# Performance work log

Measured on AMD Instinct MI355X. Metric: run time of the kernel, lower is better.

## Reference

```python
import jax, jax.numpy as jnp
import numpy as np

D_MODEL = 1024
D_STATE = 16
D_CONV = 4
EXPAND = 2
D_INNER = EXPAND * D_MODEL
BATCH = 4
SEQLEN = 2048
LN_EPS = 1e-5


def setup_inputs() -> dict:
    key = jax.random.key(0)
    ks = jax.random.split(key, 10)
    x = jax.random.normal(ks[0], (BATCH, SEQLEN, D_MODEL), dtype=jnp.float32)
    # parameters (torch Linear weights stored transposed here: [in, out])
    in_proj_w = jax.random.normal(ks[1], (D_MODEL, 2 * D_INNER), jnp.float32) * (1.0 / np.sqrt(D_MODEL))
    conv_w = jax.random.normal(ks[2], (D_INNER, 1, D_CONV), jnp.float32) * (1.0 / np.sqrt(D_CONV))  # OIH, depthwise
    conv_b = jax.random.normal(ks[3], (D_INNER,), jnp.float32) * 0.02
    x_proj_w = jax.random.normal(ks[4], (D_INNER, 2 * D_STATE), jnp.float32) * (1.0 / np.sqrt(D_INNER))
    dt_proj_w = jax.random.normal(ks[5], (D_INNER, D_INNER), jnp.float32) * (1.0 / np.sqrt(D_INNER))
    dt_proj_b = jax.random.normal(ks[6], (D_INNER,), jnp.float32) * 0.02
    # A = arange(1..d_state) repeated over d_inner; store log
    A_log = jnp.log(jnp.tile(jnp.arange(1, D_STATE + 1, dtype=jnp.float32)[None, :], (D_INNER, 1)))
    D_param = jnp.ones((D_INNER,), jnp.float32)
    out_proj_w = jax.random.normal(ks[7], (D_INNER, D_MODEL), jnp.float32) * (1.0 / np.sqrt(D_INNER))
    ln_gamma = jnp.ones((D_MODEL,), jnp.float32)
    ln_beta = jnp.zeros((D_MODEL,), jnp.float32)
    return {
        'x': x, 'ln_gamma': ln_gamma, 'ln_beta': ln_beta,
        'in_proj_w': in_proj_w, 'conv_w': conv_w, 'conv_b': conv_b,
        'x_proj_w': x_proj_w, 'dt_proj_w': dt_proj_w, 'dt_proj_b': dt_proj_b,
        'A_log': A_log, 'D_param': D_param, 'out_proj_w': out_proj_w,
    }


def _selective_scan(u, delta, A, Bm):
    # u, delta: [B, L, d_inner]; Bm: [B, L, d_state]; A: [d_inner, d_state]
    batch, _, d_inner = u.shape
    d_state = A.shape[1]

    def step(h, inp):
        u_t, d_t, b_t = inp  # [B,di], [B,di], [B,ds]
        dA = jnp.exp(d_t[..., None] * A)                      # [B,di,ds]
        h = h * dA + (u_t * d_t)[..., None] * b_t[:, None, :]  # [B,di,ds]
        return h, h.sum(-1)                                    # y_t: [B,di]

    h0 = jnp.zeros((batch, d_inner, d_state), u.dtype)
    xs = (jnp.swapaxes(u, 0, 1), jnp.swapaxes(delta, 0, 1), jnp.swapaxes(Bm, 0, 1))
    _, ys = jax.lax.scan(step, h0, xs)  # ys: [L,B,di]
    return jnp.swapaxes(ys, 0, 1)


def reference(x, ln_gamma, ln_beta, in_proj_w, conv_w, conv_b, x_proj_w,
              dt_proj_w, dt_proj_b, A_log, D_param, out_proj_w):
    residual = x
    # LayerNorm
    mu = x.mean(-1, keepdims=True)
    var = jnp.mean(jnp.square(x - mu), axis=-1, keepdims=True)
    xn = (x - mu) * jax.lax.rsqrt(var + LN_EPS) * ln_gamma + ln_beta
    # in_proj, split into u (ssm path) and z (gate)
    xz = xn @ in_proj_w                      # [B,L,2*di]
    u, z = jnp.split(xz, 2, axis=-1)
    # causal depthwise conv1d (torch pads d_conv-1 both sides then slices -> left-pad only)
    uc = jnp.swapaxes(u, 1, 2)               # [B,di,L]
    uc = jax.lax.conv_general_dilated(
        uc, conv_w, window_strides=(1,), padding=[(D_CONV - 1, 0)],
        dimension_numbers=('NCH', 'OIH', 'NCH'), feature_group_count=D_INNER,
    ) + conv_b[None, :, None]
    u = jax.nn.silu(jnp.swapaxes(uc, 1, 2))  # [B,L,di]
    # projections; note: first d_state chunk of x_dbl is discarded (overwritten by dt_proj)
    x_dbl = u @ x_proj_w                     # [B,L,2*ds]
    Bm = x_dbl[..., D_STATE:]
    delta = jax.nn.softplus(u @ dt_proj_w + dt_proj_b)
    A = -jnp.exp(A_log)
    y = _selective_scan(u, delta, A, Bm)
    y = y + u * D_param
    y = y * jax.nn.silu(z)
    return y @ out_proj_w + residual
```

## Files before the change

### kernel.cpp

```cpp
#include <hip/hip_runtime.h>

typedef unsigned short u16;
typedef unsigned int   u32;

#define D_MODEL 1024
#define D_INNER 2048
#define D_STATE 16
#define SEQLEN  2048
#define BATCH   4
#define NROWS   (BATCH*SEQLEN)
#define CHUNK   128
#define NCHUNK  (SEQLEN/CHUNK)

__device__ __forceinline__ float b2f(u16 v){
  union { u32 i; float f; } u; u.i = ((u32)v) << 16; return u.f;
}
__device__ __forceinline__ u16 f2b(float f){
  union { float f; u32 i; } u; u.f = f;
  u32 x = u.i;
  return (u16)((x + 0x7fffu + ((x >> 16) & 1u)) >> 16);
}
__device__ __forceinline__ float h2f(u16 v){
  _Float16 h; __builtin_memcpy(&h, &v, 2); return (float)h;
}
__device__ __forceinline__ u16 f2h(float f){
  _Float16 h = (_Float16)f; u16 v; __builtin_memcpy(&v, &h, 2); return v;
}

typedef __bf16 bf16x8 __attribute__((ext_vector_type(8)));
typedef float  f32x4  __attribute__((ext_vector_type(4)));

__device__ __forceinline__ void async16(u16* lds, const u16* g){
  __builtin_amdgcn_global_load_lds(
      (const __attribute__((address_space(1))) void*)g,
      (__attribute__((address_space(3))) void*)lds,
      16, 0, 0);
}

__global__ __launch_bounds__(256) void wcvt_t_kernel(
    const float* __restrict__ W, u16* __restrict__ Bt, int Kd, int Nd)
{
  __shared__ u16 tile[32][33];
  const int n0 = blockIdx.x*32, k0 = blockIdx.y*32;
  const int tx = threadIdx.x & 31, ty = threadIdx.x >> 5;
  #pragma unroll
  for (int i=0;i<32;i+=8)
    tile[ty+i][tx] = f2b(W[(size_t)(k0+ty+i)*Nd + n0+tx]);
  __syncthreads();
  #pragma unroll
  for (int i=0;i<32;i+=8)
    Bt[(size_t)(n0+ty+i)*Kd + k0+tx] = tile[tx][ty+i];
}

__global__ __launch_bounds__(256) void wxcvt_kernel(
    const float* __restrict__ Wx, u16* __restrict__ Wxt)
{
  const int k = blockIdx.x*256 + threadIdx.x;
  #pragma unroll
  for (int n=0;n<16;n++)
    Wxt[n*D_INNER + k] = f2b(Wx[(size_t)k*32 + 16 + n]);
}

__global__ __launch_bounds__(256) void ln_kernel(
    const float* __restrict__ x, const float* __restrict__ g,
    const float* __restrict__ be, u16* __restrict__ xn)
{
  const int row = blockIdx.x;
  const float* xr = x + (size_t)row * D_MODEL;
  const int tid = threadIdx.x;
  float v[4]; float s = 0.f, s2 = 0.f;
  #pragma unroll
  for (int j=0;j<4;j++){
    float f = xr[tid + 256*j];
    v[j] = f; s += f; s2 += f*f;
  }
  #pragma unroll
  for (int o=32;o>0;o>>=1){ s += __shfl_down(s,o); s2 += __shfl_down(s2,o); }
  __shared__ float sh[8];
  const int wave = tid>>6, lane = tid&63;
  if (lane==0){ sh[wave]=s; sh[4+wave]=s2; }
  __syncthreads();
  const float ts  = sh[0]+sh[1]+sh[2]+sh[3];
  const float ts2 = sh[4]+sh[5]+sh[6]+sh[7];
  const float mu  = ts * (1.f/D_MODEL);
  const float var = ts2 * (1.f/D_MODEL) - mu*mu;
  const float rstd = rsqrtf(var + 1e-5f);
  u16* xo = xn + (size_t)row * D_MODEL;
  #pragma unroll
  for (int j=0;j<4;j++){
    int i = tid + 256*j;
    xo[i] = f2b((v[j]-mu)*rstd * g[i] + be[i]);
  }
}

template<int EPI>
__global__ __launch_bounds__(256) void gemm_bk64(
    const u16* __restrict__ A, const u16* __restrict__ Bt,
    const float* __restrict__ bias, const float* __restrict__ resid,
    void* __restrict__ outv, int M, int N, int K, int gx, int gy)
{
  __shared__ __align__(16) u16 As[2*128*32];
  __shared__ __align__(16) u16 Bs[2*128*32];
  const int tid  = threadIdx.x;
  const int wave = tid >> 6, lane = tid & 63;
  const int quad = lane >> 4, l16 = lane & 15;

  const int lid = blockIdx.x;
  const int xcd = lid & 7, q = lid >> 3;
  const int cpx = gx >> 3;
  const int qd  = q / gy;
  const int bx  = xcd*cpx + qd;
  const int by  = q - qd*gy;
  const int m0 = by*128, n0 = bx*128;
  const int wm = (wave & 1)*64, wn = (wave >> 1)*64;

  const int srow = wave*32 + (lane >> 2);
  const int gcol = ((lane & 3) ^ ((lane >> 3) & 3)) * 8;
  const u16* pA = A  + (size_t)(m0 + srow)*K + gcol;
  const u16* pB = Bt + (size_t)(n0 + srow)*K + gcol;
  u16* lA = &As[(wave*32)*32];
  u16* lB = &Bs[(wave*32)*32];

  const int sw   = quad ^ ((l16 >> 1) & 3);
  const int aoff = (wm + l16)*64 + sw*16;
  const int boff = (wn + l16)*64 + sw*16;

  f32x4 acc[4][4];
  #pragma unroll
  for (int i=0;i<4;i++)
    #pragma unroll
    for (int j=0;j<4;j++) acc[i][j] = (f32x4){0.f,0.f,0.f,0.f};

  for (int k0 = 0; k0 < K; k0 += 64) {
    __syncthreads();
    async16(lA,               pA + k0);
    async16(lA + 16*32,       pA + (size_t)16*K + k0);
    async16(lA + 4096,        pA + k0 + 32);
    async16(lA + 4096+16*32,  pA + (size_t)16*K + k0 + 32);
    async16(lB,               pB + k0);
    async16(lB + 16*32,       pB + (size_t)16*K + k0);
    async16(lB + 4096,        pB + k0 + 32);
    async16(lB + 4096+16*32,  pB + (size_t)16*K + k0 + 32);
    __syncthreads();

    #pragma unroll
    for (int ks=0; ks<2; ks++){
      bf16x8 afr[4], bfr[4];
      #pragma unroll
      for (int mf=0; mf<4; mf++)
        afr[mf] = *reinterpret_cast<const bf16x8*>((const char*)As + ks*8192 + aoff + mf*1024);
      #pragma unroll
      for (int nf=0; nf<4; nf++)
        bfr[nf] = *reinterpret_cast<const bf16x8*>((const char*)Bs + ks*8192 + boff + nf*1024);
      #pragma unroll
      for (int mf=0; mf<4; mf++)
        #pragma unroll
        for (int nf=0; nf<4; nf++)
          acc[mf][nf] = __builtin_amdgcn_mfma_f32_16x16x32_bf16(afr[mf], bfr[nf], acc[mf][nf], 0, 0, 0);
    }
  }

  #pragma unroll
  for (int mf=0; mf<4; mf++){
    #pragma unroll
    for (int nf=0; nf<4; nf++){
      const int col = n0 + wn + nf*16 + l16;
      #pragma unroll
      for (int j=0;j<4;j++){
        const int row = m0 + wm + mf*16 + quad*4 + j;
        float v = acc[mf][nf][j];
        if (EPI == 1) {
          v += bias[col];
          v = (v > 20.f) ? v : log1pf(__expf(v));
          ((u16*)outv)[(size_t)row*N + col] = f2h(v);
        } else if (EPI == 2) {
          v += resid[(size_t)row*N + col];
          ((float*)outv)[(size_t)row*N + col] = v;
        } else {
          ((u16*)outv)[(size_t)row*N + col] = f2b(v);
        }
      }
    }
  }
}

__global__ __launch_bounds__(256) void conv_silu_kernel(
    const u16* __restrict__ xz, const float* __restrict__ cw,
    const float* __restrict__ cb, u16* __restrict__ u)
{
  const int idx = blockIdx.x*256 + threadIdx.x;
  const int c0 = (idx & 255) * 8;
  const int bt = idx >> 8;
  const int t  = bt & (SEQLEN-1);
  float acc[8];
  #pragma unroll
  for (int j=0;j<8;j++) acc[j] = cb[c0+j];
  #pragma unroll
  for (int k=0;k<4;k++){
    if (t - 3 + k >= 0){
      bf16x8 xv = *reinterpret_cast<const bf16x8*>(xz + (size_t)(bt-3+k)*4096 + c0);
      #pragma unroll
      for (int j=0;j<8;j++)
        acc[j] = fmaf(cw[(c0+j)*4 + k], (float)xv[j], acc[j]);
    }
  }
  u16 o[8];
  #pragma unroll
  for (int j=0;j<8;j++){
    float sv = acc[j] / (1.f + __expf(-acc[j]));
    o[j] = f2b(sv);
  }
  __builtin_memcpy(u + (size_t)bt*D_INNER + c0, o, 16);
}

__global__ __launch_bounds__(256) void xproj_kernel(
    const u16* __restrict__ u, const u16* __restrict__ Wxt, float* __restrict__ Bm)
{
  const int wave = threadIdx.x >> 6, lane = threadIdx.x & 63;
  const int m = blockIdx.x*4 + wave;
  const int n = lane & 15, kq = lane >> 4;
  const u16* ur = u   + (size_t)m*D_INNER + kq*512;
  const u16* wr = Wxt + (size_t)n*D_INNER + kq*512;
  float acc = 0.f;
  #pragma unroll 4
  for (int i=0;i<512;i+=8){
    bf16x8 uv = *reinterpret_cast<const bf16x8*>(ur + i);
    bf16x8 wv = *reinterpret_cast<const bf16x8*>(wr + i);
    #pragma unroll
    for (int j=0;j<8;j++) acc = fmaf((float)uv[j], (float)wv[j], acc);
  }
  acc += __shfl_xor(acc, 16);
  acc += __shfl_xor(acc, 32);
  if (lane < 16) Bm[(size_t)m*16 + n] = acc;
}

__global__ __launch_bounds__(256) void scan_partial(
    const u16* __restrict__ uu, const u16* __restrict__ delta16,
    const float* __restrict__ Bm, const float* __restrict__ Alog,
    float* __restrict__ hend, float* __restrict__ sumdt)
{
  const int b = blockIdx.y, ch = blockIdx.z;
  const int c = blockIdx.x*256 + threadIdx.x;
  const int row0 = b*SEQLEN + ch*CHUNK;
  float A[16], h[16];
  #pragma unroll
  for (int s=0;s<16;s++){ A[s] = -__expf(Alog[c*16+s]); h[s]=0.f; }
  __shared__ float Bsh[CHUNK*16];
  const float* src = Bm + (size_t)row0*16;
  #pragma unroll
  for (int j=0;j<8;j++) Bsh[threadIdx.x + 256*j] = src[threadIdx.x + 256*j];
  __syncthreads();

  float S = 0.f;
  float dta[8], uva[8], dtb[8], uvb[8];
  #pragma unroll
  for (int j=0;j<8;j++){
    size_t r = (size_t)(row0+j);
    dta[j] = h2f(delta16[r*D_INNER+c]);
    uva[j] = b2f(uu[r*D_INNER+c]);
  }
  #pragma unroll 1
  for (int g=0; g<CHUNK; g+=16){
    #pragma unroll
    for (int j=0;j<8;j++){
      int tl = g+8+j; tl = tl < CHUNK ? tl : CHUNK-1;
      size_t r = (size_t)(row0+tl);
      dtb[j] = h2f(delta16[r*D_INNER+c]);
      uvb[j] = b2f(uu[r*D_INNER+c]);
    }
    #pragma unroll
    for (int j=0;j<8;j++){
      float dt=dta[j], uv=uva[j]; S += dt; float xv=dt*uv;
      const float* Bt = &Bsh[(g+j)*16];
      #pragma unroll
      for (int s=0;s<16;s++) h[s] = fmaf(h[s], __expf(dt*A[s]), xv*Bt[s]);
    }
    #pragma unroll
    for (int j=0;j<8;j++){
      int tl = g+16+j; tl = tl < CHUNK ? tl : CHUNK-1;
      size_t r = (size_t)(row0+tl);
      dta[j] = h2f(delta16[r*D_INNER+c]);
      uva[j] = b2f(uu[r*D_INNER+c]);
    }
    #pragma unroll
    for (int j=0;j<8;j++){
      float dt=dtb[j], uv=uvb[j]; S += dt; float xv=dt*uv;
      const float* Bt = &Bsh[(g+8+j)*16];
      #pragma unroll
      for (int s=0;s<16;s++) h[s] = fmaf(h[s], __expf(dt*A[s]), xv*Bt[s]);
    }
  }
  const size_t base = ((size_t)(b*NCHUNK+ch)*16)*D_INNER + c;
  #pragma unroll
  for (int s=0;s<16;s++) hend[base + (size_t)s*D_INNER] = h[s];
  sumdt[(size_t)(b*NCHUNK+ch)*D_INNER + c] = S;
}

__global__ __launch_bounds__(256) void scan_combine(
    const float* __restrict__ hend, const float* __restrict__ sumdt,
    const float* __restrict__ Alog, float* __restrict__ hin)
{
  const int b = blockIdx.y;
  const int c = blockIdx.x*256 + threadIdx.x;
  float A[16], h[16];
  #pragma unroll
  for (int s=0;s<16;s++){ A[s] = -__expf(Alog[c*16+s]); h[s]=0.f; }
  #pragma unroll 1
  for (int k=0;k<NCHUNK;k++){
    const size_t base = ((size_t)(b*NCHUNK+k)*16)*D_INNER + c;
    #pragma unroll
    for (int s=0;s<16;s++) hin[base + (size_t)s*D_INNER] = h[s];
    const float S = sumdt[(size_t)(b*NCHUNK+k)*D_INNER + c];
    #pragma unroll
    for (int s=0;s<16;s++)
      h[s] = fmaf(h[s], __expf(S*A[s]), hend[base + (size_t)s*D_INNER]);
  }
}

__global__ __launch_bounds__(256) void scan_final(
    const u16* __restrict__ uu, const u16* __restrict__ delta16,
    const float* __restrict__ Bm, const u16* __restrict__ xz,
    const float* __restrict__ Alog, const float* __restrict__ Dpar,
    const float* __restrict__ hin, u16* __restrict__ yg)
{
  const int b = blockIdx.y, ch = blockIdx.z;
  const int c = blockIdx.x*256 + threadIdx.x;
  const int row0 = b*SEQLEN + ch*CHUNK;
  float A[16], h[16];
  const size_t base = ((size_t)(b*NCHUNK+ch)*16)*D_INNER + c;
  #pragma unroll
  for (int s=0;s<16;s++){
    A[s] = -__expf(Alog[c*16+s]);
    h[s] = hin[base + (size_t)s*D_INNER];
  }
  const float Dc = Dpar[c];
  __shared__ float Bsh[CHUNK*16];
  const float* src = Bm + (size_t)row0*16;
  #pragma unroll
  for (int j=0;j<8;j++) Bsh[threadIdx.x + 256*j] = src[threadIdx.x + 256*j];
  __syncthreads();

  float dta[8], uva[8], zva[8], dtb[8], uvb[8], zvb[8];
  #pragma unroll
  for (int j=0;j<8;j++){
    size_t r = (size_t)(row0+j);
    dta[j] = h2f(delta16[r*D_INNER+c]);
    uva[j] = b2f(uu[r*D_INNER+c]);
    zva[j] = b2f(xz[r*4096 + D_INNER + c]);
  }
  #pragma unroll 1
  for (int g=0; g<CHUNK; g+=16){
    #pragma unroll
    for (int j=0;j<8;j++){
      int tl = g+8+j; tl = tl < CHUNK ? tl : CHUNK-1;
      size_t r = (size_t)(row0+tl);
      dtb[j] = h2f(delta16[r*D_INNER+c]);
      uvb[j] = b2f(uu[r*D_INNER+c]);
      zvb[j] = b2f(xz[r*4096 + D_INNER + c]);
    }
    #pragma unroll
    for (int j=0;j<8;j++){
      float dt=dta[j], uv=uva[j], zv=zva[j];
      float xv=dt*uv, y=0.f;
      const float* Bt = &Bsh[(g+j)*16];
      #pragma unroll
      for (int s=0;s<16;s++){
        h[s] = fmaf(h[s], __expf(dt*A[s]), xv*Bt[s]);
        y += h[s];
      }
      y = fmaf(uv, Dc, y);
      float gz = zv/(1.f+__expf(-zv));
      yg[(size_t)(row0+g+j)*D_INNER + c] = f2b(y*gz);
    }
    #pragma unroll
    for (int j=0;j<8;j++){
      int tl = g+16+j; tl = tl < CHUNK ? tl : CHUNK-1;
      size_t r = (size_t)(row0+tl);
      dta[j] = h2f(delta16[r*D_INNER+c]);
      uva[j] = b2f(uu[r*D_INNER+c]);
      zva[j] = b2f(xz[r*4096 + D_INNER + c]);
    }
    #pragma unroll
    for (int j=0;j<8;j++){
      float dt=dtb[j], uv=uvb[j], zv=zvb[j];
      float xv=dt*uv, y=0.f;
      const float* Bt = &Bsh[(g+8+j)*16];
      #pragma unroll
      for (int s=0;s<16;s++){
        h[s] = fmaf(h[s], __expf(dt*A[s]), xv*Bt[s]);
        y += h[s];
      }
      y = fmaf(uv, Dc, y);
      float gz = zv/(1.f+__expf(-zv));
      yg[(size_t)(row0+g+8+j)*D_INNER + c] = f2b(y*gz);
    }
  }
}

extern "C" void kernel_launch(void* const* d_in, const int* in_sizes, int n_in,
                              void* d_out, int out_size, void* d_ws, size_t ws_size,
                              hipStream_t stream)
{
  const float* x    = (const float*)d_in[0];
  const float* lng  = (const float*)d_in[1];
  const float* lnb  = (const float*)d_in[2];
  const float* W1   = (const float*)d_in[3];
  const float* cw   = (const float*)d_in[4];
  const float* cb   = (const float*)d_in[5];
  const float* Wx   = (const float*)d_in[6];
  const float* Wdt  = (const float*)d_in[7];
  const float* dtb  = (const float*)d_in[8];
  const float* Alog = (const float*)d_in[9];
  const float* Dpar = (const float*)d_in[10];
  const float* Wout = (const float*)d_in[11];

  char* ws = (char*)d_ws;
  u16*   dlt   = (u16*)(ws);
  u16*   xn    = (u16*)(ws);
  u16*   xz    = (u16*)(ws + (32llu<<20));
  u16*   uu    = (u16*)(ws + (96llu<<20));
  float* Bm    = (float*)(ws + (128llu<<20));
  u16*   W1t   = (u16*)(ws + (129llu<<20));
  u16*   Wdtt  = (u16*)(ws + (137llu<<20));
  u16*   Woutt = (u16*)(ws + (145llu<<20));
  u16*   yg    = (u16*)(ws + (149llu<<20));
  float* hend  = (float*)(ws + (181llu<<20));
  float* sumdt = (float*)(ws + (189llu<<20));
  float* hin   = (float*)(ws + (190llu<<20));
  u16*   Wxt   = (u16*)(ws + (198llu<<20));

  wcvt_t_kernel<<<dim3(2*D_INNER/32, D_MODEL/32), 256, 0, stream>>>(W1,  W1t,  D_MODEL, 2*D_INNER);
  wcvt_t_kernel<<<dim3(D_INNER/32,  D_INNER/32), 256, 0, stream>>>(Wdt, Wdtt, D_INNER, D_INNER);
  wcvt_t_kernel<<<dim3(D_MODEL/32,  D_INNER/32), 256, 0, stream>>>(Wout,Woutt,D_INNER, D_MODEL);
  wxcvt_kernel<<<D_INNER/256, 256, 0, stream>>>(Wx, Wxt);

  ln_kernel<<<NROWS, 256, 0, stream>>>(x, lng, lnb, xn);

  {
    const int gx = 2*D_INNER/128, gy = NROWS/128;
    gemm_bk64<0><<<gx*gy, 256, 0, stream>>>(
        xn, W1t, nullptr, nullptr, (void*)xz, NROWS, 2*D_INNER, D_MODEL, gx, gy);
  }

  conv_silu_kernel<<<(NROWS*D_INNER/8)/256, 256, 0, stream>>>(xz, cw, cb, uu);

  xproj_kernel<<<NROWS/4, 256, 0, stream>>>(uu, Wxt, Bm);

  {
    const int gx = D_INNER/128, gy = NROWS/128;
    gemm_bk64<1><<<gx*gy, 256, 0, stream>>>(
        uu, Wdtt, dtb, nullptr, (void*)dlt, NROWS, D_INNER, D_INNER, gx, gy);
  }

  scan_partial<<<dim3(D_INNER/256, BATCH, NCHUNK), 256, 0, stream>>>(
      uu, dlt, Bm, Alog, hend, sumdt);
  scan_combine<<<dim3(D_INNER/256, BATCH), 256, 0, stream>>>(
      hend, sumdt, Alog, hin);
  scan_final<<<dim3(D_INNER/256, BATCH, NCHUNK), 256, 0, stream>>>(
      uu, dlt, Bm, xz, Alog, Dpar, hin, yg);

  {
    const int gx = D_MODEL/128, gy = NROWS/128;
    gemm_bk64<2><<<gx*gy, 256, 0, stream>>>(
        yg, Woutt, nullptr, x, d_out, NROWS, D_MODEL, D_INNER, gx, gy);
  }

  (void)in_sizes; (void)n_in; (void)out_size; (void)ws_size;
}
```

Baseline: 783.3 us.

## Replace 128x128 GEMM with 256x256 tile, 4-stage async pipelined kernel

Replaces the double-sync 128x128 bf16 MFMA GEMM with a 256x256 tile, 512-thread kernel. It uses a 4-deep ring of LDS buffers filled by async global-to-LDS loads issued three k-steps ahead, with s_setprio around MFMA bursts and split A-fragment loads to interleave LDS reads with compute. The goal is to raise data reuse per tile and hide global memory latency behind MFMA work. The cost is larger LDS use (128KB), lower occupancy, and fewer blocks for the smaller GEMMs (128 blocks for out_proj), which may underfill the GPU.

```diff
diff --git a/kernel.cpp b/kernel.cpp
--- a/kernel.cpp
+++ b/kernel.cpp
@@ -94,80 +94,124 @@
 }
 
 template<int EPI>
-__global__ __launch_bounds__(256) void gemm_bk64(
+__global__ __launch_bounds__(512) void gemm256(
     const u16* __restrict__ A, const u16* __restrict__ Bt,
     const float* __restrict__ bias, const float* __restrict__ resid,
     void* __restrict__ outv, int M, int N, int K, int gx, int gy)
 {
-  __shared__ __align__(16) u16 As[2*128*32];
-  __shared__ __align__(16) u16 Bs[2*128*32];
+  __shared__ __align__(16) u16 As[4*8192];
+  __shared__ __align__(16) u16 Bs[4*8192];
   const int tid  = threadIdx.x;
   const int wave = tid >> 6, lane = tid & 63;
   const int quad = lane >> 4, l16 = lane & 15;
+  const int wm = wave >> 2, wn = wave & 3;
 
   const int lid = blockIdx.x;
-  const int xcd = lid & 7, q = lid >> 3;
-  const int cpx = gx >> 3;
-  const int qd  = q / gy;
-  const int bx  = xcd*cpx + qd;
-  const int by  = q - qd*gy;
-  const int m0 = by*128, n0 = bx*128;
-  const int wm = (wave & 1)*64, wn = (wave >> 1)*64;
-
-  const int srow = wave*32 + (lane >> 2);
-  const int gcol = ((lane & 3) ^ ((lane >> 3) & 3)) * 8;
-  const u16* pA = A  + (size_t)(m0 + srow)*K + gcol;
-  const u16* pB = Bt + (size_t)(n0 + srow)*K + gcol;
-  u16* lA = &As[(wave*32)*32];
-  u16* lB = &Bs[(wave*32)*32];
-
-  const int sw   = quad ^ ((l16 >> 1) & 3);
-  const int aoff = (wm + l16)*64 + sw*16;
-  const int boff = (wn + l16)*64 + sw*16;
-
-  f32x4 acc[4][4];
-  #pragma unroll
-  for (int i=0;i<4;i++)
+  int bx, by;
+  if ((gx & 7) == 0) {
+    const int xcd = lid & 7, q = lid >> 3;
+    const int cpx = gx >> 3;
+    const int qd  = q / gy;
+    bx = xcd*cpx + qd;
+    by = q - qd*gy;
+  } else {
+    bx = lid / gy;
+    by = lid - bx*gy;
+  }
+  const int m0 = by*256, n0 = bx*256;
+
+  const int gl   = (tid & 3) ^ ((tid >> 3) & 3);
+  const int srow = tid >> 2;
+  const u16* sA0 = A  + (size_t)(m0 + srow)*K       + gl*8;
+  const u16* sA1 = A  + (size_t)(m0 + 128 + srow)*K + gl*8;
+  const u16* sB0 = Bt + (size_t)(n0 + srow)*K       + gl*8;
+  const u16* sB1 = Bt + (size_t)(n0 + 128 + srow)*K + gl*8;
+  u16* dA = As + wave*512;
+  u16* dB = Bs + wave*512;
+
+  const int swz = quad ^ ((l16 >> 1) & 3);
+  const char* aBase = (const char*)As + (wm*128 + l16)*64 + swz*16;
+  const char* bBase = (const char*)Bs + (wn*64  + l16)*64 + swz*16;
+
+  f32x4 acc[8][4];
+  #pragma unroll
+  for (int i=0;i<8;i++)
     #pragma unroll
     for (int j=0;j<4;j++) acc[i][j] = (f32x4){0.f,0.f,0.f,0.f};
 
-  for (int k0 = 0; k0 < K; k0 += 64) {
-    __syncthreads();
-    async16(lA,               pA + k0);
-    async16(lA + 16*32,       pA + (size_t)16*K + k0);
-    async16(lA + 4096,        pA + k0 + 32);
-    async16(lA + 4096+16*32,  pA + (size_t)16*K + k0 + 32);
-    async16(lB,               pB + k0);
-    async16(lB + 16*32,       pB + (size_t)16*K + k0);
-    async16(lB + 4096,        pB + k0 + 32);
-    async16(lB + 4096+16*32,  pB + (size_t)16*K + k0 + 32);
-    __syncthreads();
-
-    #pragma unroll
-    for (int ks=0; ks<2; ks++){
-      bf16x8 afr[4], bfr[4];
-      #pragma unroll
-      for (int mf=0; mf<4; mf++)
-        afr[mf] = *reinterpret_cast<const bf16x8*>((const char*)As + ks*8192 + aoff + mf*1024);
-      #pragma unroll
-      for (int nf=0; nf<4; nf++)
-        bfr[nf] = *reinterpret_cast<const bf16x8*>((const char*)Bs + ks*8192 + boff + nf*1024);
-      #pragma unroll
-      for (int mf=0; mf<4; mf++)
-        #pragma unroll
-        for (int nf=0; nf<4; nf++)
-          acc[mf][nf] = __builtin_amdgcn_mfma_f32_16x16x32_bf16(afr[mf], bfr[nf], acc[mf][nf], 0, 0, 0);
-    }
-  }
-
-  #pragma unroll
-  for (int mf=0; mf<4; mf++){
+  const int KT = K >> 5;
+
+  #pragma unroll
+  for (int p=0;p<3;p++){
+    const int ko = p*32;
+    u16* da = dA + p*8192; u16* db = dB + p*8192;
+    async16(da,        sA0 + ko);
+    async16(da + 4096, sA1 + ko);
+    async16(db,        sB0 + ko);
+    async16(db + 4096, sB1 + ko);
+  }
+  asm volatile("s_waitcnt vmcnt(8)" ::: "memory");
+  __builtin_amdgcn_s_barrier();
+  __builtin_amdgcn_sched_barrier(0);
+
+  for (int kt = 0; kt < KT; ++kt){
+    const int c = kt & 3;
+    const char* aT = aBase + c*16384;
+    const char* bT = bBase + c*16384;
+
+    bf16x8 af[4], bfr[4];
+    #pragma unroll
+    for (int mf=0;mf<4;mf++) af[mf]  = *(const bf16x8*)(aT + mf*1024);
+    #pragma unroll
+    for (int nf=0;nf<4;nf++) bfr[nf] = *(const bf16x8*)(bT + nf*1024);
+    {
+      int k3 = kt + 3; k3 = (k3 < KT) ? k3 : (KT-1);
+      const int b3 = (kt + 3) & 3;
+      const int ko = k3*32;
+      u16* da = dA + b3*8192; u16* db = dB + b3*8192;
+      async16(da,        sA0 + ko);
+      async16(da + 4096, sA1 + ko);
+      async16(db,        sB0 + ko);
+      async16(db + 4096, sB1 + ko);
+    }
+    __builtin_amdgcn_s_barrier();
+    asm volatile("s_waitcnt lgkmcnt(0)" ::: "memory");
+    __builtin_amdgcn_sched_barrier(0);
+    __builtin_amdgcn_s_setprio(1);
+    #pragma unroll
+    for (int mf=0;mf<4;mf++)
+      #pragma unroll
+      for (int nf=0;nf<4;nf++)
+        acc[mf][nf] = __builtin_amdgcn_mfma_f32_16x16x32_bf16(af[mf], bfr[nf], acc[mf][nf], 0, 0, 0);
+    __builtin_amdgcn_s_setprio(0);
+    __builtin_amdgcn_s_barrier();
+
+    bf16x8 ag[4];
+    #pragma unroll
+    for (int mf=0;mf<4;mf++) ag[mf] = *(const bf16x8*)(aT + (4+mf)*1024);
+    __builtin_amdgcn_s_barrier();
+    asm volatile("s_waitcnt lgkmcnt(0)" ::: "memory");
+    __builtin_amdgcn_sched_barrier(0);
+    __builtin_amdgcn_s_setprio(1);
+    #pragma unroll
+    for (int mf=0;mf<4;mf++)
+      #pragma unroll
+      for (int nf=0;nf<4;nf++)
+        acc[4+mf][nf] = __builtin_amdgcn_mfma_f32_16x16x32_bf16(ag[mf], bfr[nf], acc[4+mf][nf], 0, 0, 0);
+    __builtin_amdgcn_s_setprio(0);
+    asm volatile("s_waitcnt vmcnt(8)" ::: "memory");
+    __builtin_amdgcn_s_barrier();
+    __builtin_amdgcn_sched_barrier(0);
+  }
+
+  #pragma unroll
+  for (int mf=0; mf<8; mf++){
     #pragma unroll
     for (int nf=0; nf<4; nf++){
-      const int col = n0 + wn + nf*16 + l16;
+      const int col = n0 + wn*64 + nf*16 + l16;
       #pragma unroll
       for (int j=0;j<4;j++){
-        const int row = m0 + wm + mf*16 + quad*4 + j;
+        const int row = m0 + wm*128 + mf*16 + quad*4 + j;
         float v = acc[mf][nf][j];
         if (EPI == 1) {
           v += bias[col];
@@ -437,8 +481,8 @@
   ln_kernel<<<NROWS, 256, 0, stream>>>(x, lng, lnb, xn);
 
   {
-    const int gx = 2*D_INNER/128, gy = NROWS/128;
-    gemm_bk64<0><<<gx*gy, 256, 0, stream>>>(
+    const int gx = 2*D_INNER/256, gy = NROWS/256;
+    gemm256<0><<<gx*gy, 512, 0, stream>>>(
         xn, W1t, nullptr, nullptr, (void*)xz, NROWS, 2*D_INNER, D_MODEL, gx, gy);
   }
 
@@ -447,8 +491,8 @@
   xproj_kernel<<<NROWS/4, 256, 0, stream>>>(uu, Wxt, Bm);
 
   {
-    const int gx = D_INNER/128, gy = NROWS/128;
-    gemm_bk64<1><<<gx*gy, 256, 0, stream>>>(
+    const int gx = D_INNER/256, gy = NROWS/256;
+    gemm256<1><<<gx*gy, 512, 0, stream>>>(
         uu, Wdtt, dtb, nullptr, (void*)dlt, NROWS, D_INNER, D_INNER, gx, gy);
   }
 
@@ -460,8 +504,8 @@
       uu, dlt, Bm, xz, Alog, Dpar, hin, yg);
 
   {
-    const int gx = D_MODEL/128, gy = NROWS/128;
-    gemm_bk64<2><<<gx*gy, 256, 0, stream>>>(
+    const int gx = D_MODEL/256, gy = NROWS/256;
+    gemm256<2><<<gx*gy, 512, 0, stream>>>(
         yg, Woutt, nullptr, x, d_out, NROWS, D_MODEL, D_INNER, gx, gy);
   }
 
```

New measurement: 777.5 us. About the same (-0.7%).
